# Optimization experiments

Hardware: AMD Instinct MI355X
Metric: run time of the kernel (lower is better)

Reference implementation:

```python
import jax, jax.numpy as jnp
import numpy as np

B, D, C = 512, 16384, 3
SAMPLE_DURATION = 16
NEG_THRESHOLD = 0.5
NEGPOS_RATIO = 3


def setup_inputs() -> dict:
    key = jax.random.key(0)
    k1, k2, k3, k4, k5, k6, k7 = jax.random.split(key, 7)
    loc_pred = jax.random.normal(k1, (B, D, 2), dtype=jnp.float32)
    conf_pred = jax.random.normal(k2, (B, D, C), dtype=jnp.float32)
    # one ground-truth (start, end, label) per sample, within [0, 16]
    start = jax.random.uniform(k3, (B,), dtype=jnp.float32) * 8.0
    length = 1.0 + jax.random.uniform(k4, (B,), dtype=jnp.float32) * 7.0
    label = jax.random.randint(k5, (B,), 0, C).astype(jnp.float32)
    targets = jnp.stack([start, start + length, label], axis=-1)  # [B,3]
    # default bars stored as (center, length) in frame units
    centers = 1.0 + jax.random.uniform(k6, (D,), dtype=jnp.float32) * (SAMPLE_DURATION - 2.0)
    lengths = 1.0 + jax.random.uniform(k7, (D,), dtype=jnp.float32) * (SAMPLE_DURATION - 4.0)
    default_bar = jnp.stack([centers, lengths], axis=-1)  # [D,2]
    return {"loc_pred": loc_pred, "conf_pred": conf_pred,
            "targets": targets, "default_bar": default_bar}


def _match_one(truth, label, default):
    """truth [2]=(start,end), label scalar int, default [D,2]=(center,length).
    Returns loc_t [D,2], conf_t [D] (0=ignore, 1=background, >1=fg)."""
    d_c, d_l = default[:, 0], default[:, 1]
    d_s, d_e = d_c - d_l * 0.5, d_c + d_l * 0.5
    inter = jnp.clip(jnp.minimum(truth[1], d_e) - jnp.maximum(truth[0], d_s), 0.0)
    union = (truth[1] - truth[0]) + (d_e - d_s) - inter
    ov = inter / union                                   # [D] 1-D IoU
    best_prior = jnp.argmax(ov)                          # best anchor for the truth
    bto = ov.at[best_prior].set(2.0)                     # index_fill_ with 2
    conf = jnp.full((D,), label + 1, dtype=jnp.int32)    # single truth -> broadcast
    is_bg = conf == 1
    conf = jnp.where(bto < NEG_THRESHOLD, 0, conf)
    conf = jnp.where(is_bg, 1, conf)
    # SSD-style encoding of matched (start,end) against (center,length)
    m_c = (truth[0] + truth[1]) * 0.5
    m_l = truth[1] - truth[0]
    loc = jnp.stack([(m_c - d_c) / d_l, jnp.log(m_l / d_l)], axis=-1)  # [D,2]
    return loc, conf


def reference(loc_pred, conf_pred, targets, default_bar):
    truths = targets[:, :2]                              # [B,2]
    labels = targets[:, 2].astype(jnp.int32)             # [B]
    loc_t, conf_t = jax.vmap(_match_one, in_axes=(0, 0, None))(truths, labels, default_bar)
    loc_t = jax.lax.stop_gradient(loc_t)                 # built under no_grad in torch
    conf_t = jax.lax.stop_gradient(conf_t)

    pos = conf_t > 0                                     # [B,D] used for mining
    loc_pos = conf_t > 1                                 # [B,D] used for loc loss

    # SmoothL1 (beta=1), reduction='sum' over positives
    diff = loc_pred - loc_t
    ad = jnp.abs(diff)
    sl1 = jnp.where(ad < 1.0, 0.5 * diff * diff, ad - 0.5)
    loss_loc = jnp.sum(sl1 * loc_pos[..., None].astype(sl1.dtype))

    # hard-negative mining on per-anchor CE surrogate
    conf_tc = jnp.clip(conf_t - 1, 0)                    # [B,D] class ids 0..C-1
    lse = jax.nn.logsumexp(conf_pred, axis=-1)           # [B,D]
    gathered = jnp.take_along_axis(conf_pred, conf_tc[..., None], axis=-1)[..., 0]
    lc = lse - gathered
    lc = jnp.where(pos, 0.0, lc)
    loss_idx = jnp.argsort(-lc, axis=1)                  # descending sort
    idx_rank = jnp.argsort(loss_idx, axis=1)
    num_pos = jnp.sum(pos.astype(jnp.int32), axis=1, keepdims=True)   # [B,1]
    num_neg = jnp.clip(NEGPOS_RATIO * num_pos, max=D - 1)
    neg = idx_rank < num_neg                             # [B,D]

    sel = (pos | neg).astype(conf_pred.dtype)
    logp = jax.nn.log_softmax(conf_pred, axis=-1)
    ce = -jnp.take_along_axis(logp, conf_tc[..., None], axis=-1)[..., 0]
    loss_conf = jnp.sum(ce * sel)

    N = jnp.sum(num_pos).astype(loss_loc.dtype)
    return jnp.stack([loss_loc / N, loss_conf / N])
```

## Files before the change

### kernel.cpp

```cpp
#include <hip/hip_runtime.h>
#include <hip/hip_fp16.h>
#include <math.h>

constexpr int Bn = 512;
constexpr int Dn = 16384;
constexpr int BS = 512;
constexpr int CHUNKS = 32;
constexpr int CPRI = Dn / CHUNKS;
constexpr int K1T = 256;

__device__ __forceinline__ float lse3(float a, float b, float c) {
  float m = fmaxf(a, fmaxf(b, c));
  return m + __logf(__expf(a - m) + __expf(b - m) + __expf(c - m));
}
__device__ __forceinline__ float sl1f(float x) {
  float a = fabsf(x);
  return a < 1.f ? 0.5f * x * x : a - 0.5f;
}

__device__ __forceinline__ double blockReduceAddD(double v, double* sred) {
  int t = threadIdx.x;
  sred[t] = v;
  __syncthreads();
  for (int off = BS >> 1; off > 0; off >>= 1) {
    if (t < off) sred[t] += sred[t + off];
    __syncthreads();
  }
  double r = sred[0];
  __syncthreads();
  return r;
}

__global__ __launch_bounds__(K1T) void multiloss_stream(
    const float* __restrict__ loc_pred, const float* __restrict__ conf_pred,
    const float* __restrict__ targets, const float* __restrict__ default_bar,
    unsigned* __restrict__ lc32,
    float* __restrict__ pce, float* __restrict__ plloc, int* __restrict__ pnpos)
{
  __shared__ float s_conf[CPRI * 3];
  __shared__ float s_bar[CPRI * 2];
  __shared__ float s_red[12];

  const int bid = blockIdx.x;
  const int b = bid >> 5, c = bid & 31;
  const int t = threadIdx.x;
  const int l = t & 63, w = t >> 6;
  const int wb = t & ~63;

  {
    const float4* srcC = (const float4*)(conf_pred + (size_t)b * Dn * 3) + (size_t)c * (CPRI * 3 / 4);
    float4* dstC = (float4*)s_conf;
    __builtin_amdgcn_global_load_lds(
        (const __attribute__((address_space(1))) void*)(srcC + t),
        (__attribute__((address_space(3))) void*)(dstC + wb), 16, 0, 0);
    if (t < 128)
      __builtin_amdgcn_global_load_lds(
          (const __attribute__((address_space(1))) void*)(srcC + 256 + t),
          (__attribute__((address_space(3))) void*)(dstC + 256 + wb), 16, 0, 0);
    const float4* srcB = (const float4*)default_bar + (size_t)c * (CPRI * 2 / 4);
    float4* dstB = (float4*)s_bar;
    __builtin_amdgcn_global_load_lds(
        (const __attribute__((address_space(1))) void*)(srcB + t),
        (__attribute__((address_space(3))) void*)(dstB + wb), 16, 0, 0);
  }

  const float t0  = targets[b * 3 + 0];
  const float t1  = targets[b * 3 + 1];
  const int   lab = (int)targets[b * 3 + 2];

  float ce = 0.f, lloc = 0.f; int npos = 0;
  const float m_c = (t0 + t1) * 0.5f;
  const float T   = t1 - t0;

  __syncthreads();

  const float2 ca  = ((const float2*)s_conf)[3 * t];
  const float2 cb  = ((const float2*)s_conf)[3 * t + 1];
  const float2 cc_ = ((const float2*)s_conf)[3 * t + 2];

  if (lab == 0) {
    {
      float hi = fmaxf(ca.x, ca.y), lo = fminf(ca.x, ca.y);
      float m  = fmaxf(hi, cb.x),  mid = fminf(hi, cb.x);
      float s  = 1.f + __expf(lo - m) + __expf(mid - m);
      ce += (m - ca.x) + __logf(s);
    }
    {
      float hi = fmaxf(cb.y, cc_.x), lo = fminf(cb.y, cc_.x);
      float m  = fmaxf(hi, cc_.y),  mid = fminf(hi, cc_.y);
      float s  = 1.f + __expf(lo - m) + __expf(mid - m);
      ce += (m - cb.y) + __logf(s);
    }
  } else {
    const float log_ml = __logf(T);
    const float2* __restrict__ lp2 = (const float2*)loc_pred + (size_t)b * Dn + (size_t)c * CPRI;
    const float4 bb = ((const float4*)s_bar)[t];
    float lcv0, lcv1;
    const int pA = 2 * t;

    {
      float dc = bb.x, dl = bb.y;
      float ds = __fmaf_rn(-0.5f, dl, dc);
      float de = __fmaf_rn(0.5f, dl, dc);
      float inter = fmaxf(fminf(t1, de) - fmaxf(t0, ds), 0.f);
      float uni = (T + dl) - inter;
      bool pos = (2.f * inter >= uni);
      float hi = fmaxf(ca.x, ca.y), lo = fminf(ca.x, ca.y);
      float m  = fmaxf(hi, cb.x),  mid = fminf(hi, cb.x);
      float s  = 1.f + __expf(lo - m) + __expf(mid - m);
      float lnS = __logf(s);
      float cl = (lab == 1) ? ca.y : cb.x;
      npos += pos;
      ce += pos ? ((m - cl) + lnS) : 0.f;
      lcv0 = pos ? 0.f : ((m - ca.x) + lnS);
      if (pos) {
        float2 lp = lp2[pA];
        float pd0 = lp.x - __fdividef(m_c - dc, dl);
        float pd1 = (lp.y - log_ml) + __logf(dl);
        lloc += sl1f(pd0) + sl1f(pd1);
      }
    }
    {
      float dc = bb.z, dl = bb.w;
      float ds = __fmaf_rn(-0.5f, dl, dc);
      float de = __fmaf_rn(0.5f, dl, dc);
      float inter = fmaxf(fminf(t1, de) - fmaxf(t0, ds), 0.f);
      float uni = (T + dl) - inter;
      bool pos = (2.f * inter >= uni);
      float hi = fmaxf(cb.y, cc_.x), lo = fminf(cb.y, cc_.x);
      float m  = fmaxf(hi, cc_.y),  mid = fminf(hi, cc_.y);
      float s  = 1.f + __expf(lo - m) + __expf(mid - m);
      float lnS = __logf(s);
      float cl = (lab == 1) ? cc_.x : cc_.y;
      npos += pos;
      ce += pos ? ((m - cl) + lnS) : 0.f;
      lcv1 = pos ? 0.f : ((m - cb.y) + lnS);
      if (pos) {
        float2 lp = lp2[pA + 1];
        float pd0 = lp.x - __fdividef(m_c - dc, dl);
        float pd1 = (lp.y - log_ml) + __logf(dl);
        lloc += sl1f(pd0) + sl1f(pd1);
      }
    }
    __half2 hv = __floats2half2_rn(lcv0, lcv1);
    unsigned* lcrow = lc32 + ((size_t)b * Dn + (size_t)c * CPRI) / 2;
    lcrow[t] = *reinterpret_cast<unsigned*>(&hv);
  }

  #pragma unroll
  for (int off = 1; off < 64; off <<= 1) {
    ce   += __shfl_xor(ce, off);
    lloc += __shfl_xor(lloc, off);
    npos += __shfl_xor(npos, off);
  }
  if (l == 0) {
    s_red[w * 3 + 0] = ce; s_red[w * 3 + 1] = lloc; s_red[w * 3 + 2] = __int_as_float(npos);
  }
  __syncthreads();
  if (t == 0) {
    float Ce = 0.f, Ll = 0.f; int Np = 0;
    #pragma unroll
    for (int k = 0; k < 4; ++k) {
      Ce += s_red[k * 3 + 0]; Ll += s_red[k * 3 + 1]; Np += __float_as_int(s_red[k * 3 + 2]);
    }
    int pidx = b * CHUNKS + c;
    pce[pidx] = Ce; plloc[pidx] = Ll; pnpos[pidx] = Np;
  }
}

__global__ __launch_bounds__(BS) void multiloss_select(
    const float* __restrict__ loc_pred, const float* __restrict__ conf_pred,
    const float* __restrict__ targets, const float* __restrict__ default_bar,
    const unsigned short* __restrict__ lc16,
    const float* __restrict__ pce, const float* __restrict__ plloc,
    const int* __restrict__ pnpos,
    double* __restrict__ rloc, double* __restrict__ rconf, double* __restrict__ rnp)
{
  __shared__ unsigned short s_lc[Dn];
  __shared__ int      s_hist[256];
  __shared__ double   s_dred[BS];
  __shared__ float    s_fv[BS];
  __shared__ int      s_fi[BS];
  __shared__ unsigned s_wt[8];
  __shared__ unsigned s_sel[2];
  __shared__ double   s_sc[2];
  __shared__ int      s_np;

  const int b = blockIdx.x;
  const int t = threadIdx.x;
  const int lab = (int)targets[b * 3 + 2];

  if (lab == 0) {
    if (t == 0) {
      double ce = 0.0;
      for (int kk = 0; kk < CHUNKS; ++kk) ce += (double)pce[CHUNKS * b + kk];
      rloc[b] = 0.0; rconf[b] = ce; rnp[b] = (double)Dn;
    }
    return;
  }

  const float t0 = targets[b * 3 + 0];
  const float t1 = targets[b * 3 + 1];

  const float4* lcr = (const float4*)(lc16 + (size_t)b * Dn);
  float4* sl4 = (float4*)s_lc;
  #pragma unroll
  for (int j = 0; j < Dn / 8 / BS; ++j) sl4[j * BS + t] = lcr[j * BS + t];
  __syncthreads();

  if (t == 0) {
    double ce = 0.0, ll = 0.0; int np = 0;
    for (int kk = 0; kk < CHUNKS; ++kk) {
      int pi = CHUNKS * b + kk;
      ce += (double)pce[pi]; ll += (double)plloc[pi]; np += pnpos[pi];
    }
    s_sc[0] = ce; s_sc[1] = ll; s_np = np;
  }
  __syncthreads();
  int np = s_np;

  if (np == 0) {
    float bV = -1.f; int bI = 0;
    for (int d = t; d < Dn; d += BS) {
      float2 db = ((const float2*)default_bar)[d];
      float d_s = db.x - db.y * 0.5f;
      float d_e = db.x + db.y * 0.5f;
      float inter = fmaxf(fminf(t1, d_e) - fmaxf(t0, d_s), 0.f);
      float uni = (t1 - t0) + (d_e - d_s) - inter;
      float ov = inter / uni;
      if (ov > bV) { bV = ov; bI = d; }
    }
    s_fv[t] = bV; s_fi[t] = bI;
    __syncthreads();
    for (int off = BS >> 1; off > 0; off >>= 1) {
      if (t < off) {
        float v2 = s_fv[t + off]; int i2 = s_fi[t + off];
        if (v2 > s_fv[t] || (v2 == s_fv[t] && i2 < s_fi[t])) { s_fv[t] = v2; s_fi[t] = i2; }
      }
      __syncthreads();
    }
    if (t == 0) {
      int d = s_fi[0];
      const float* cp = conf_pred + (size_t)b * Dn * 3 + (size_t)d * 3;
      float c0 = cp[0], c1 = cp[1], c2 = cp[2];
      float lse = lse3(c0, c1, c2);
      float cl = (lab == 1) ? c1 : c2;
      float2 db = ((const float2*)default_bar)[d];
      float2 lp = ((const float2*)loc_pred)[(size_t)b * Dn + d];
      float m_c = (t0 + t1) * 0.5f, m_l = t1 - t0;
      float pd0 = lp.x - (m_c - db.x) / db.y;
      float pd1 = lp.y - __logf(m_l / db.y);
      s_sc[0] += (double)(lse - cl);
      s_sc[1] += (double)(sl1f(pd0) + sl1f(pd1));
      s_np = 1;
      s_lc[d] = 0;
    }
    __syncthreads();
    np = s_np;
  }
  const int k = min(3 * np, Dn - 1);

  unsigned prefix = 0;
  int K = k;
  const int lane = t & 63, w = t >> 6;
  for (int r = 0; r < 2; ++r) {
    if (t < 256) s_hist[t] = 0;
    __syncthreads();
    for (int d = t; d < Dn; d += BS) {
      unsigned u = s_lc[d];
      bool ok = (r == 0) || ((u >> 8) == prefix);
      if (ok) {
        unsigned bin = (r == 0) ? (u >> 8) : (u & 0xFFu);
        atomicAdd(&s_hist[bin], 1);
      }
    }
    __syncthreads();
    unsigned psum = (t < 256) ? (unsigned)s_hist[t] : 0u;
    unsigned incl = psum;
    #pragma unroll
    for (int off = 1; off < 64; off <<= 1) {
      unsigned v = __shfl_down(incl, off, 64);
      if (lane + off < 64) incl += v;
    }
    if (lane == 0) s_wt[w] = incl;
    __syncthreads();
    unsigned aboveW = 0;
    for (int w2 = w + 1; w2 < 8; ++w2) aboveW += s_wt[w2];
    const unsigned above = aboveW + (incl - psum);
    if (t < 256 && above < (unsigned)K && (unsigned)K <= above + psum) {
      s_sel[0] = (unsigned)t;
      s_sel[1] = above;
    }
    __syncthreads();
    unsigned selBin = s_sel[0];
    K -= (int)s_sel[1];
    prefix = (r == 0) ? selBin : ((prefix << 8) | selBin);
    __syncthreads();
  }
  const unsigned tb = prefix;

  float    ssum = 0.f;
  unsigned scnt = 0;
  for (int d = t; d < Dn; d += BS) {
    unsigned u = s_lc[d];
    if (u > tb) {
      ssum += __half2float(__ushort_as_half((unsigned short)u));
      scnt++;
    }
  }
  double S = blockReduceAddD((double)ssum, s_dred);
  double C = blockReduceAddD((double)scnt, s_dred);

  if (t == 0) {
    double tval = (double)__half2float(__ushort_as_half((unsigned short)tb));
    double topk = S + ((double)k - C) * tval;
    rloc[b]  = s_sc[1];
    rconf[b] = s_sc[0] + topk;
    rnp[b]   = (double)np;
  }
}

__global__ __launch_bounds__(BS) void multiloss_mono(
    const float* __restrict__ loc_pred, const float* __restrict__ conf_pred,
    const float* __restrict__ targets, const float* __restrict__ default_bar,
    double* __restrict__ rloc, double* __restrict__ rconf, double* __restrict__ rnp)
{
  __shared__ float    s_lc[Dn];
  __shared__ int      s_hist[2048];
  __shared__ unsigned s_scan[BS];
  __shared__ double   s_dred[BS];
  __shared__ unsigned s_sel[2];
  __shared__ double   s_corr[2];
  __shared__ int      s_np;

  const int b = blockIdx.x;
  const int t = threadIdx.x;

  const float t0  = targets[b * 3 + 0];
  const float t1  = targets[b * 3 + 1];
  const int   lab = (int)targets[b * 3 + 2];

  const float* __restrict__ cpb = conf_pred + (size_t)b * Dn * 3;

  if (lab == 0) {
    float ce = 0.f;
    for (int d = t; d < Dn; d += BS) {
      const float* cp = cpb + d * 3;
      ce += lse3(cp[0], cp[1], cp[2]) - cp[0];
    }
    double tot = blockReduceAddD((double)ce, s_dred);
    if (t == 0) { rloc[b] = 0.0; rconf[b] = tot; rnp[b] = (double)Dn; }
    return;
  }

  const float m_c = (t0 + t1) * 0.5f;
  const float m_l = t1 - t0;

  float bestV = -1.f; int bestI = 0;
  int   nposL = 0;
  float cePosL = 0.f;
  float llocL  = 0.f;

  for (int d = t; d < Dn; d += BS) {
    float2 db = ((const float2*)default_bar)[d];
    float d_c = db.x, d_l = db.y;
    float d_s = d_c - d_l * 0.5f;
    float d_e = d_c + d_l * 0.5f;
    float inter = fmaxf(fminf(t1, d_e) - fmaxf(t0, d_s), 0.f);
    float uni = (t1 - t0) + (d_e - d_s) - inter;
    float ov  = inter / uni;

    const float* cp = cpb + d * 3;
    float c0 = cp[0];
    float lse = lse3(cp[0], cp[1], cp[2]);

    if (ov > bestV) { bestV = ov; bestI = d; }

    float lcv;
    if (ov >= 0.5f) {
      nposL++;
      float cl = (lab == 1) ? cp[1] : cp[2];
      cePosL += lse - cl;
      float2 lp = ((const float2*)loc_pred)[(size_t)b * Dn + d];
      float pd0 = lp.x - (m_c - d_c) / d_l;
      float pd1 = lp.y - __logf(m_l / d_l);
      llocL += sl1f(pd0) + sl1f(pd1);
      lcv = 0.f;
    } else {
      lcv = lse - c0;
    }
    s_lc[d] = lcv;
  }

  float* sv = (float*)s_hist;
  int*   si = (int*)(s_hist + BS);
  sv[t] = bestV; si[t] = bestI;
  __syncthreads();
  for (int off = BS >> 1; off > 0; off >>= 1) {
    if (t < off) {
      float v2 = sv[t + off]; int i2 = si[t + off];
      if (v2 > sv[t] || (v2 == sv[t] && i2 < si[t])) { sv[t] = v2; si[t] = i2; }
    }
    __syncthreads();
  }
  float bV = sv[0]; int bI = si[0];
  __syncthreads();

  double nposTot  = blockReduceAddD((double)nposL, s_dred);
  double cePosTot = blockReduceAddD((double)cePosL, s_dred);
  double llocTot  = blockReduceAddD((double)llocL, s_dred);
  int num_pos = (int)(nposTot + 0.5);

  if (t == 0) {
    double cc = 0.0, lcor = 0.0; int np2 = num_pos;
    if (bV < 0.5f) {
      int d = bI;
      const float* cp = cpb + d * 3;
      float lse = lse3(cp[0], cp[1], cp[2]);
      float cl = (lab == 1) ? cp[1] : cp[2];
      cc = (double)(lse - cl);
      float2 db = ((const float2*)default_bar)[d];
      float2 lp = ((const float2*)loc_pred)[(size_t)b * Dn + d];
      float pd0 = lp.x - (m_c - db.x) / db.y;
      float pd1 = lp.y - __logf(m_l / db.y);
      lcor = (double)(sl1f(pd0) + sl1f(pd1));
      np2 += 1;
      s_lc[d] = 0.f;
    }
    s_corr[0] = cc; s_corr[1] = lcor; s_np = np2;
  }
  __syncthreads();
  int np = s_np;
  int k  = min(3 * np, Dn - 1);

  unsigned prefix = 0;
  int K = k;
  for (int r = 0; r < 3; ++r) {
    for (int i = t; i < 2048; i += BS) s_hist[i] = 0;
    __syncthreads();
    for (int d = t; d < Dn; d += BS) {
      unsigned u = __float_as_uint(s_lc[d]);
      bool ok = (r == 0) || (r == 1 ? ((u >> 21) == prefix) : ((u >> 10) == prefix));
      if (ok) {
        unsigned bin = (r == 0) ? (u >> 21)
                     : (r == 1) ? ((u >> 10) & 0x7FFu)
                                : (u & 0x3FFu);
        atomicAdd(&s_hist[bin], 1);
      }
    }
    __syncthreads();
    int nb  = (r == 2) ? 1024 : 2048;
    int per = nb / BS;
    unsigned psum = 0;
    for (int j = 0; j < per; ++j) psum += (unsigned)s_hist[t * per + j];
    s_scan[t] = psum;
    __syncthreads();
    for (int off = 1; off < BS; off <<= 1) {
      unsigned v = (t + off < BS) ? s_scan[t + off] : 0u;
      __syncthreads();
      s_scan[t] += v;
      __syncthreads();
    }
    unsigned above = (t < BS - 1) ? s_scan[t + 1] : 0u;
    if (above < (unsigned)K && (unsigned)K <= above + psum) {
      unsigned cum = above;
      int found = 0;
      for (int j = per - 1; j >= 0; --j) {
        unsigned c = (unsigned)s_hist[t * per + j];
        if (cum + c >= (unsigned)K) { found = j; break; }
        cum += c;
      }
      s_sel[0] = (unsigned)(t * per + found);
      s_sel[1] = cum;
    }
    __syncthreads();
    unsigned selBin = s_sel[0];
    K -= (int)s_sel[1];
    prefix = (r == 0) ? selBin
           : (r == 1) ? ((prefix << 11) | selBin)
                      : ((prefix << 10) | selBin);
    __syncthreads();
  }
  const unsigned tb = prefix;

  float    ssum = 0.f;
  unsigned scnt = 0;
  for (int d = t; d < Dn; d += BS) {
    float v = s_lc[d];
    if (__float_as_uint(v) > tb) { ssum += v; scnt++; }
  }
  double S = blockReduceAddD((double)ssum, s_dred);
  double C = blockReduceAddD((double)scnt, s_dred);

  if (t == 0) {
    double tval = (double)__uint_as_float(tb);
    double topk = S + ((double)k - C) * tval;
    rloc[b]  = llocTot + s_corr[1];
    rconf[b] = cePosTot + s_corr[0] + topk;
    rnp[b]   = (double)s_np;
  }
}

__global__ __launch_bounds__(512) void multiloss_final(
    const double* __restrict__ rloc, const double* __restrict__ rconf,
    const double* __restrict__ rnp, float* __restrict__ out)
{
  __shared__ double s1[512], s2[512], s3[512];
  int t = threadIdx.x;
  s1[t] = rloc[t];
  s2[t] = rconf[t];
  s3[t] = rnp[t];
  __syncthreads();
  for (int off = 256; off > 0; off >>= 1) {
    if (t < off) { s1[t] += s1[t + off]; s2[t] += s2[t + off]; s3[t] += s3[t + off]; }
    __syncthreads();
  }
  if (t == 0) {
    double N = s3[0];
    out[0] = (float)(s1[0] / N);
    out[1] = (float)(s2[0] / N);
  }
}

extern "C" void kernel_launch(void* const* d_in, const int* in_sizes, int n_in,
                              void* d_out, int out_size, void* d_ws, size_t ws_size,
                              hipStream_t stream) {
  const float* loc_pred    = (const float*)d_in[0];
  const float* conf_pred   = (const float*)d_in[1];
  const float* targets     = (const float*)d_in[2];
  const float* default_bar = (const float*)d_in[3];
  float* out = (float*)d_out;
  char* ws = (char*)d_ws;

  constexpr size_t LC_BYTES = (size_t)Bn * Dn * sizeof(unsigned short);
  constexpr size_t P_CNT = (size_t)Bn * CHUNKS;
  size_t off = LC_BYTES;
  float*  pce   = (float*)(ws + off); off += P_CNT * 4;
  float*  plloc = (float*)(ws + off); off += P_CNT * 4;
  int*    pnpos = (int*)(ws + off);   off += P_CNT * 4;
  double* rloc  = (double*)(ws + off); off += Bn * 8;
  double* rconf = (double*)(ws + off); off += Bn * 8;
  double* rnp   = (double*)(ws + off); off += Bn * 8;
  const size_t NEED = off;

  if (ws_size >= NEED) {
    hipLaunchKernelGGL(multiloss_stream, dim3(Bn * CHUNKS), dim3(K1T), 0, stream,
                       loc_pred, conf_pred, targets, default_bar,
                       (unsigned*)ws, pce, plloc, pnpos);
    hipLaunchKernelGGL(multiloss_select, dim3(Bn), dim3(BS), 0, stream,
                       loc_pred, conf_pred, targets, default_bar,
                       (const unsigned short*)ws, pce, plloc, pnpos,
                       rloc, rconf, rnp);
    hipLaunchKernelGGL(multiloss_final, dim3(1), dim3(512), 0, stream,
                       rloc, rconf, rnp, out);
  } else {
    double* mloc  = (double*)ws;
    double* mconf = mloc + Bn;
    double* mnp   = mconf + Bn;
    hipLaunchKernelGGL(multiloss_mono, dim3(Bn), dim3(BS), 0, stream,
                       loc_pred, conf_pred, targets, default_bar, mloc, mconf, mnp);
    hipLaunchKernelGGL(multiloss_final, dim3(1), dim3(512), 0, stream,
                       mloc, mconf, mnp, out);
  }
}
```

Baseline: 60.79 us.

## Double-buffer per-wave LDS staging in stream kernel with fewer, larger blocks

Cuts the per-row chunk count from 32 to 4 so each block handles 4096 anchors. Each wave now streams four tiles through two LDS buffers using async global-to-LDS loads and explicit vmcnt/lgkmcnt waits, overlapping loads with compute. The aim is to lower per-block launch and sync overhead and hide memory latency. In exchange there are fewer blocks for occupancy and fragile hand-counted waitcnt values.

After: 63.44 us. 1.04x slower.

```diff
diff --git a/kernel.cpp b/kernel.cpp
--- a/kernel.cpp
+++ b/kernel.cpp
@@ -5,9 +5,11 @@
 constexpr int Bn = 512;
 constexpr int Dn = 16384;
 constexpr int BS = 512;
-constexpr int CHUNKS = 32;
+constexpr int CHUNKS = 4;
 constexpr int CPRI = Dn / CHUNKS;
 constexpr int K1T = 256;
+constexpr int WT = 4;
+constexpr int TP = 256;
 
 __device__ __forceinline__ float lse3(float a, float b, float c) {
   float m = fmaxf(a, fmaxf(b, c));
@@ -30,6 +32,11 @@
   __syncthreads();
   return r;
 }
+
+#define WAITV(n) do { asm volatile("s_waitcnt vmcnt(" #n ")" ::: "memory"); \
+                      __builtin_amdgcn_sched_barrier(0); } while (0)
+#define WAITL()  do { asm volatile("s_waitcnt lgkmcnt(0)" ::: "memory"); \
+                      __builtin_amdgcn_sched_barrier(0); } while (0)
 
 __global__ __launch_bounds__(K1T) void multiloss_stream(
     const float* __restrict__ loc_pred, const float* __restrict__ conf_pred,
@@ -37,32 +44,39 @@
     unsigned* __restrict__ lc32,
     float* __restrict__ pce, float* __restrict__ plloc, int* __restrict__ pnpos)
 {
-  __shared__ float s_conf[CPRI * 3];
-  __shared__ float s_bar[CPRI * 2];
-  __shared__ float s_red[12];
+  __shared__ float s_lds[4 * 2 * 1280];
 
   const int bid = blockIdx.x;
-  const int b = bid >> 5, c = bid & 31;
+  const int b = bid >> 2, c = bid & 3;
   const int t = threadIdx.x;
   const int l = t & 63, w = t >> 6;
-  const int wb = t & ~63;
-
-  {
-    const float4* srcC = (const float4*)(conf_pred + (size_t)b * Dn * 3) + (size_t)c * (CPRI * 3 / 4);
-    float4* dstC = (float4*)s_conf;
-    __builtin_amdgcn_global_load_lds(
-        (const __attribute__((address_space(1))) void*)(srcC + t),
-        (__attribute__((address_space(3))) void*)(dstC + wb), 16, 0, 0);
-    if (t < 128)
+
+  float4* wbuf = (float4*)(s_lds + w * 2560);
+
+  const float4* __restrict__ confs =
+      (const float4*)conf_pred + (size_t)b * 12288 + c * 3072 + w * 768;
+  const float4* __restrict__ bars =
+      (const float4*)default_bar + c * 2048 + w * 512;
+
+  auto stage = [&](int buf, int tile) {
+    const float4* cs = confs + tile * 192;
+    float4* cd = wbuf + buf * 320;
+    #pragma unroll
+    for (int j = 0; j < 3; ++j)
       __builtin_amdgcn_global_load_lds(
-          (const __attribute__((address_space(1))) void*)(srcC + 256 + t),
-          (__attribute__((address_space(3))) void*)(dstC + 256 + wb), 16, 0, 0);
-    const float4* srcB = (const float4*)default_bar + (size_t)c * (CPRI * 2 / 4);
-    float4* dstB = (float4*)s_bar;
-    __builtin_amdgcn_global_load_lds(
-        (const __attribute__((address_space(1))) void*)(srcB + t),
-        (__attribute__((address_space(3))) void*)(dstB + wb), 16, 0, 0);
-  }
+          (const __attribute__((address_space(1))) void*)(cs + j * 64 + l),
+          (__attribute__((address_space(3))) void*)(cd + j * 64), 16, 0, 0);
+    const float4* bs = bars + tile * 128;
+    float4* bd = cd + 192;
+    #pragma unroll
+    for (int j = 0; j < 2; ++j)
+      __builtin_amdgcn_global_load_lds(
+          (const __attribute__((address_space(1))) void*)(bs + j * 64 + l),
+          (__attribute__((address_space(3))) void*)(bd + j * 64), 16, 0, 0);
+  };
+
+  stage(0, 0);
+  stage(1, 1);
 
   const float t0  = targets[b * 3 + 0];
   const float t1  = targets[b * 3 + 1];
@@ -72,79 +86,73 @@
   const float m_c = (t0 + t1) * 0.5f;
   const float T   = t1 - t0;
 
-  __syncthreads();
-
-  const float2 ca  = ((const float2*)s_conf)[3 * t];
-  const float2 cb  = ((const float2*)s_conf)[3 * t + 1];
-  const float2 cc_ = ((const float2*)s_conf)[3 * t + 2];
-
   if (lab == 0) {
-    {
-      float hi = fmaxf(ca.x, ca.y), lo = fminf(ca.x, ca.y);
-      float m  = fmaxf(hi, cb.x),  mid = fminf(hi, cb.x);
-      float s  = 1.f + __expf(lo - m) + __expf(mid - m);
-      ce += (m - ca.x) + __logf(s);
-    }
-    {
-      float hi = fmaxf(cb.y, cc_.x), lo = fminf(cb.y, cc_.x);
-      float m  = fmaxf(hi, cc_.y),  mid = fminf(hi, cc_.y);
-      float s  = 1.f + __expf(lo - m) + __expf(mid - m);
-      ce += (m - cb.y) + __logf(s);
-    }
+    auto consume0 = [&](int buf) {
+      const float4* cd = wbuf + buf * 320;
+      float4 cA = cd[3 * l], cB = cd[3 * l + 1], cC = cd[3 * l + 2];
+      const float cf[12] = {cA.x, cA.y, cA.z, cA.w, cB.x, cB.y, cB.z, cB.w, cC.x, cC.y, cC.z, cC.w};
+      #pragma unroll
+      for (int i = 0; i < 4; ++i) {
+        float x = cf[3 * i], y = cf[3 * i + 1], z = cf[3 * i + 2];
+        float hi = fmaxf(x, y), lo = fminf(x, y);
+        float m  = fmaxf(hi, z), mid = fminf(hi, z);
+        float s  = 1.f + __expf(lo - m) + __expf(mid - m);
+        ce += (m - x) + __logf(s);
+      }
+    };
+    WAITV(5); consume0(0); WAITL(); stage(0, 2);
+    WAITV(5); consume0(1); WAITL(); stage(1, 3);
+    WAITV(5); consume0(0);
+    WAITV(0); consume0(1);
   } else {
     const float log_ml = __logf(T);
-    const float2* __restrict__ lp2 = (const float2*)loc_pred + (size_t)b * Dn + (size_t)c * CPRI;
-    const float4 bb = ((const float4*)s_bar)[t];
-    float lcv0, lcv1;
-    const int pA = 2 * t;
-
-    {
-      float dc = bb.x, dl = bb.y;
-      float ds = __fmaf_rn(-0.5f, dl, dc);
-      float de = __fmaf_rn(0.5f, dl, dc);
-      float inter = fmaxf(fminf(t1, de) - fmaxf(t0, ds), 0.f);
-      float uni = (T + dl) - inter;
-      bool pos = (2.f * inter >= uni);
-      float hi = fmaxf(ca.x, ca.y), lo = fminf(ca.x, ca.y);
-      float m  = fmaxf(hi, cb.x),  mid = fminf(hi, cb.x);
-      float s  = 1.f + __expf(lo - m) + __expf(mid - m);
-      float lnS = __logf(s);
-      float cl = (lab == 1) ? ca.y : cb.x;
-      npos += pos;
-      ce += pos ? ((m - cl) + lnS) : 0.f;
-      lcv0 = pos ? 0.f : ((m - ca.x) + lnS);
-      if (pos) {
-        float2 lp = lp2[pA];
-        float pd0 = lp.x - __fdividef(m_c - dc, dl);
-        float pd1 = (lp.y - log_ml) + __logf(dl);
-        lloc += sl1f(pd0) + sl1f(pd1);
+    const float2* __restrict__ lp2 =
+        (const float2*)loc_pred + (size_t)b * Dn + c * CPRI + w * 1024;
+    unsigned* __restrict__ lcbase = lc32 + (size_t)b * 8192 + (c * CPRI + w * 1024) / 2;
+
+    auto consume = [&](int buf, int tile) {
+      const float4* cd = wbuf + buf * 320;
+      const float4* bd = cd + 192;
+      float4 cA = cd[3 * l], cB = cd[3 * l + 1], cC = cd[3 * l + 2];
+      float4 b0 = bd[2 * l], b1 = bd[2 * l + 1];
+      const float cf[12] = {cA.x, cA.y, cA.z, cA.w, cB.x, cB.y, cB.z, cB.w, cC.x, cC.y, cC.z, cC.w};
+      const float bf[8]  = {b0.x, b0.y, b0.z, b0.w, b1.x, b1.y, b1.z, b1.w};
+      float lcv[4];
+      const int gbase = tile * TP + 4 * l;
+      #pragma unroll
+      for (int i = 0; i < 4; ++i) {
+        float x = cf[3 * i], y = cf[3 * i + 1], z = cf[3 * i + 2];
+        float dc = bf[2 * i], dl = bf[2 * i + 1];
+        float ds = __fmaf_rn(-0.5f, dl, dc);
+        float de = __fmaf_rn(0.5f, dl, dc);
+        float inter = fmaxf(fminf(t1, de) - fmaxf(t0, ds), 0.f);
+        float uni = (T + dl) - inter;
+        bool pos = (2.f * inter >= uni);
+        float hi = fmaxf(x, y), lo = fminf(x, y);
+        float m  = fmaxf(hi, z), mid = fminf(hi, z);
+        float s  = 1.f + __expf(lo - m) + __expf(mid - m);
+        float lnS = __logf(s);
+        float cl = (lab == 1) ? y : z;
+        npos += pos;
+        ce += pos ? ((m - cl) + lnS) : 0.f;
+        lcv[i] = pos ? 0.f : ((m - x) + lnS);
+        if (pos) {
+          float2 lp = lp2[gbase + i];
+          float pd0 = lp.x - __fdividef(m_c - dc, dl);
+          float pd1 = (lp.y - log_ml) + __logf(dl);
+          lloc += sl1f(pd0) + sl1f(pd1);
+        }
       }
-    }
-    {
-      float dc = bb.z, dl = bb.w;
-      float ds = __fmaf_rn(-0.5f, dl, dc);
-      float de = __fmaf_rn(0.5f, dl, dc);
-      float inter = fmaxf(fminf(t1, de) - fmaxf(t0, ds), 0.f);
-      float uni = (T + dl) - inter;
-      bool pos = (2.f * inter >= uni);
-      float hi = fmaxf(cb.y, cc_.x), lo = fminf(cb.y, cc_.x);
-      float m  = fmaxf(hi, cc_.y),  mid = fminf(hi, cc_.y);
-      float s  = 1.f + __expf(lo - m) + __expf(mid - m);
-      float lnS = __logf(s);
-      float cl = (lab == 1) ? cc_.x : cc_.y;
-      npos += pos;
-      ce += pos ? ((m - cl) + lnS) : 0.f;
-      lcv1 = pos ? 0.f : ((m - cb.y) + lnS);
-      if (pos) {
-        float2 lp = lp2[pA + 1];
-        float pd0 = lp.x - __fdividef(m_c - dc, dl);
-        float pd1 = (lp.y - log_ml) + __logf(dl);
-        lloc += sl1f(pd0) + sl1f(pd1);
-      }
-    }
-    __half2 hv = __floats2half2_rn(lcv0, lcv1);
-    unsigned* lcrow = lc32 + ((size_t)b * Dn + (size_t)c * CPRI) / 2;
-    lcrow[t] = *reinterpret_cast<unsigned*>(&hv);
+      __half2 h0 = __floats2half2_rn(lcv[0], lcv[1]);
+      __half2 h1 = __floats2half2_rn(lcv[2], lcv[3]);
+      uint2 pk = make_uint2(*reinterpret_cast<unsigned*>(&h0),
+                            *reinterpret_cast<unsigned*>(&h1));
+      ((uint2*)(lcbase + tile * (TP / 2)))[l] = pk;
+    };
+    WAITV(5); consume(0, 0); WAITL(); stage(0, 2);
+    WAITV(6); consume(1, 1); WAITL(); stage(1, 3);
+    WAITV(6); consume(0, 2);
+    WAITV(1); consume(1, 3);
   }
 
   #pragma unroll
@@ -153,15 +161,17 @@
     lloc += __shfl_xor(lloc, off);
     npos += __shfl_xor(npos, off);
   }
+  __syncthreads();
+  float* red = s_lds;
   if (l == 0) {
-    s_red[w * 3 + 0] = ce; s_red[w * 3 + 1] = lloc; s_red[w * 3 + 2] = __int_as_float(npos);
+    red[w * 3 + 0] = ce; red[w * 3 + 1] = lloc; red[w * 3 + 2] = __int_as_float(npos);
   }
   __syncthreads();
   if (t == 0) {
     float Ce = 0.f, Ll = 0.f; int Np = 0;
     #pragma unroll
     for (int k = 0; k < 4; ++k) {
-      Ce += s_red[k * 3 + 0]; Ll += s_red[k * 3 + 1]; Np += __float_as_int(s_red[k * 3 + 2]);
+      Ce += red[k * 3 + 0]; Ll += red[k * 3 + 1]; Np += __float_as_int(red[k * 3 + 2]);
     }
     int pidx = b * CHUNKS + c;
     pce[pidx] = Ce; plloc[pidx] = Ll; pnpos[pidx] = Np;
```
